# Optimization experiments

Measured on AMD Instinct MI355X. Metric: run time of the kernel, lower is better.

The kernel has to match this reference:

```python
import jax, jax.numpy as jnp
import numpy as np

N = 8192
F = 64
OUT = 64


def setup_inputs() -> dict:
    key = jax.random.key(0)
    k1, k2, k3 = jax.random.split(key, 3)
    adj = jax.random.uniform(k1, (N, N), dtype=jnp.float32)
    features = jax.random.normal(k2, (N, F), dtype=jnp.float32)
    # torch Linear weight: [out_features, in_features*2], xavier_uniform with relu gain
    gain = float(np.sqrt(2.0))
    fan_in, fan_out = 2 * F, OUT
    bound = gain * float(np.sqrt(6.0 / (fan_in + fan_out)))
    W = jax.random.uniform(k3, (OUT, 2 * F), dtype=jnp.float32, minval=-bound, maxval=bound)
    return {"adj": adj, "features": features, "W": W}


def reference(adj, features, W):
    # neigh = (adj @ x) / (rowsum(adj) + 1)   -- dense 2D branch of SageConvLayer
    deg = jnp.sum(adj, axis=1, keepdims=True) + 1.0          # [N, 1]
    neigh = jnp.matmul(adj, features) / deg                   # [N, F]
    data = jnp.concatenate([features, neigh], axis=-1)        # [N, 2F]
    return jnp.matmul(data, W.T)                              # [N, OUT]
```

## Files before the change

### kernel.cpp

```cpp
#include <hip/hip_runtime.h>

#define NN 8192
#define FF 64
#define NOUT 64
#define KS 16
#define KCHUNK (NN / KS)

typedef __bf16 bf16x8 __attribute__((ext_vector_type(8)));
typedef float f32x4 __attribute__((ext_vector_type(4)));

__device__ inline bf16x8 cvt8(float4 a, float4 b) {
    bf16x8 r;
    r[0] = (__bf16)a.x; r[1] = (__bf16)a.y; r[2] = (__bf16)a.z; r[3] = (__bf16)a.w;
    r[4] = (__bf16)b.x; r[5] = (__bf16)b.y; r[6] = (__bf16)b.z; r[7] = (__bf16)b.w;
    return r;
}

__global__ __launch_bounds__(256)
void transpose_kernel(const float* __restrict__ feat, __bf16* __restrict__ featT) {
    __shared__ __bf16 t[64][72];
    int tid = threadIdx.x, blk = blockIdx.x;
    int r = tid >> 2, c0 = (tid & 3) * 16;
    const float* p = feat + (size_t)(blk * 64 + r) * FF + c0;
    float4 v0 = *(const float4*)(p);
    float4 v1 = *(const float4*)(p + 4);
    float4 v2 = *(const float4*)(p + 8);
    float4 v3 = *(const float4*)(p + 12);
    #pragma unroll
    for (int j = 0; j < 4; ++j) {
        t[c0 + 0 + j][r]  = (__bf16)(&v0.x)[j];
        t[c0 + 4 + j][r]  = (__bf16)(&v1.x)[j];
        t[c0 + 8 + j][r]  = (__bf16)(&v2.x)[j];
        t[c0 + 12 + j][r] = (__bf16)(&v3.x)[j];
    }
    __syncthreads();
    int n = tid >> 2, co = (tid & 3) * 16;
    __bf16* dst = featT + (size_t)n * NN + blk * 64 + co;
    *(bf16x8*)dst       = *(const bf16x8*)&t[n][co];
    *(bf16x8*)(dst + 8) = *(const bf16x8*)&t[n][co + 8];
}

__global__ __launch_bounds__(256, 4)
void main_kernel(const float* __restrict__ adj, const __bf16* __restrict__ featT,
                 __bf16* __restrict__ partN, float* __restrict__ partDeg) {
    int tid = threadIdx.x;
    int w = tid >> 6, lane = tid & 63, ln = lane & 15, q = lane >> 4;
    int ks = blockIdx.x & (KS - 1);
    int mt = blockIdx.x >> 4;

    int rowA = mt * 128 + w * 32 + ln;
    const float*  ap0 = adj + (size_t)rowA * NN + ks * KCHUNK + q * 8;
    const float*  ap1 = ap0 + (size_t)16 * NN;
    const __bf16* bp  = featT + (size_t)ln * NN + ks * KCHUNK + q * 8;

    f32x4 acc[2][4], accd[2];
    #pragma unroll
    for (int f = 0; f < 2; ++f) {
        accd[f] = 0;
        #pragma unroll
        for (int t = 0; t < 4; ++t) acc[f][t] = 0;
    }

    bf16x8 ones;
    __bf16 o = (ln == 0) ? (__bf16)1.0f : (__bf16)0.0f;
    #pragma unroll
    for (int i = 0; i < 8; ++i) ones[i] = o;

    #pragma unroll 2
    for (int it = 0; it < KCHUNK / 32; ++it) {
        float4 a0 = *(const float4*)ap0;
        float4 a1 = *(const float4*)(ap0 + 4);
        float4 a2 = *(const float4*)ap1;
        float4 a3 = *(const float4*)(ap1 + 4);
        bf16x8 b0 = *(const bf16x8*)(bp);
        bf16x8 b1 = *(const bf16x8*)(bp + 16 * NN);
        bf16x8 b2 = *(const bf16x8*)(bp + 32 * NN);
        bf16x8 b3 = *(const bf16x8*)(bp + 48 * NN);
        bf16x8 af0 = cvt8(a0, a1);
        bf16x8 af1 = cvt8(a2, a3);
        acc[0][0] = __builtin_amdgcn_mfma_f32_16x16x32_bf16(af0, b0, acc[0][0], 0, 0, 0);
        acc[1][0] = __builtin_amdgcn_mfma_f32_16x16x32_bf16(af1, b0, acc[1][0], 0, 0, 0);
        acc[0][1] = __builtin_amdgcn_mfma_f32_16x16x32_bf16(af0, b1, acc[0][1], 0, 0, 0);
        acc[1][1] = __builtin_amdgcn_mfma_f32_16x16x32_bf16(af1, b1, acc[1][1], 0, 0, 0);
        acc[0][2] = __builtin_amdgcn_mfma_f32_16x16x32_bf16(af0, b2, acc[0][2], 0, 0, 0);
        acc[1][2] = __builtin_amdgcn_mfma_f32_16x16x32_bf16(af1, b2, acc[1][2], 0, 0, 0);
        acc[0][3] = __builtin_amdgcn_mfma_f32_16x16x32_bf16(af0, b3, acc[0][3], 0, 0, 0);
        acc[1][3] = __builtin_amdgcn_mfma_f32_16x16x32_bf16(af1, b3, acc[1][3], 0, 0, 0);
        accd[0] = __builtin_amdgcn_mfma_f32_16x16x32_bf16(af0, ones, accd[0], 0, 0, 0);
        accd[1] = __builtin_amdgcn_mfma_f32_16x16x32_bf16(af1, ones, accd[1], 0, 0, 0);
        ap0 += 32; ap1 += 32; bp += 32;
    }

    #pragma unroll
    for (int f = 0; f < 2; ++f) {
        int grow = mt * 128 + w * 32 + f * 16 + q * 4;
        #pragma unroll
        for (int r = 0; r < 4; ++r) {
            size_t base = ((size_t)(ks << 13) + grow + r) * FF + ln;
            partN[base +  0] = (__bf16)acc[f][0][r];
            partN[base + 16] = (__bf16)acc[f][1][r];
            partN[base + 32] = (__bf16)acc[f][2][r];
            partN[base + 48] = (__bf16)acc[f][3][r];
        }
        if (ln == 0) {
            #pragma unroll
            for (int r = 0; r < 4; ++r)
                partDeg[(ks << 13) + grow + r] = accd[f][r];
        }
    }
}

__global__ __launch_bounds__(256)
void epilogue_kernel(const float* __restrict__ feat, const float* __restrict__ W,
                     const __bf16* __restrict__ partN, const float* __restrict__ partDeg,
                     float* __restrict__ out) {
    __shared__ __bf16 dataB[64][136];
    __shared__ float rdeg[64];
    int tid = threadIdx.x, blk = blockIdx.x;

    if (tid < 64) {
        float s = 0.f;
        #pragma unroll
        for (int ks = 0; ks < KS; ++ks) s += partDeg[(ks << 13) + blk * 64 + tid];
        rdeg[tid] = 1.0f / (s + 1.0f);
    }
    __syncthreads();

    #pragma unroll
    for (int i = 0; i < 2; ++i) {
        int idx = tid + i * 256;
        int r = idx >> 3, c = (idx & 7) * 8;
        float s[8];
        #pragma unroll
        for (int j = 0; j < 8; ++j) s[j] = 0.f;
        #pragma unroll
        for (int ks = 0; ks < KS; ++ks) {
            bf16x8 v = *(const bf16x8*)&partN[((size_t)(ks << 13) + blk * 64 + r) * FF + c];
            #pragma unroll
            for (int j = 0; j < 8; ++j) s[j] += (float)v[j];
        }
        float rd = rdeg[r];
        bf16x8 o;
        #pragma unroll
        for (int j = 0; j < 8; ++j) o[j] = (__bf16)(s[j] * rd);
        *(bf16x8*)&dataB[r][64 + c] = o;
    }
    #pragma unroll
    for (int i = 0; i < 2; ++i) {
        int idx = tid + i * 256;
        int r = idx >> 3, c = (idx & 7) * 8;
        const float* p = feat + (size_t)(blk * 64 + r) * FF + c;
        float4 f0 = *(const float4*)p;
        float4 f1 = *(const float4*)(p + 4);
        *(bf16x8*)&dataB[r][c] = cvt8(f0, f1);
    }
    __syncthreads();

    int w = tid >> 6, lane = tid & 63, ln = lane & 15, q = lane >> 4;
    f32x4 acc[4];
    #pragma unroll
    for (int t = 0; t < 4; ++t) acc[t] = 0;

    #pragma unroll
    for (int kk = 0; kk < 4; ++kk) {
        bf16x8 af = *(const bf16x8*)&dataB[w * 16 + ln][kk * 32 + q * 8];
        #pragma unroll
        for (int t = 0; t < 4; ++t) {
            const float* wp = W + (size_t)(t * 16 + ln) * 128 + kk * 32 + q * 8;
            float4 b0 = *(const float4*)wp;
            float4 b1 = *(const float4*)(wp + 4);
            bf16x8 bf = cvt8(b0, b1);
            acc[t] = __builtin_amdgcn_mfma_f32_16x16x32_bf16(af, bf, acc[t], 0, 0, 0);
        }
    }

    int grow = blk * 64 + w * 16 + q * 4;
    #pragma unroll
    for (int t = 0; t < 4; ++t)
        #pragma unroll
        for (int r = 0; r < 4; ++r)
            out[(size_t)(grow + r) * NOUT + t * 16 + ln] = acc[t][r];
}

extern "C" void kernel_launch(void* const* d_in, const int* in_sizes, int n_in,
                              void* d_out, int out_size, void* d_ws, size_t ws_size,
                              hipStream_t stream) {
    const float* adj  = (const float*)d_in[0];
    const float* feat = (const float*)d_in[1];
    const float* W    = (const float*)d_in[2];
    float* out = (float*)d_out;
    char* ws = (char*)d_ws;

    __bf16* featT   = (__bf16*)ws;
    __bf16* partN   = (__bf16*)(ws + (1 << 20));
    float*  partDeg = (float*)(ws + (1 << 20) + (size_t)KS * NN * FF * 2);

    transpose_kernel<<<NN / 64, 256, 0, stream>>>(feat, featT);
    main_kernel<<<(NN / 128) * KS, 256, 0, stream>>>(adj, featT, partN, partDeg);
    epilogue_kernel<<<NN / 64, 256, 0, stream>>>(feat, W, partN, partDeg, out);
}
```

Baseline: 381.0 us.

## Stage adj tiles through LDS with coalesced row loads before MFMA

The main kernel now loads adj in coalesced 16-lane row segments (64 floats per row per round), converts them to bf16 and writes them into a shared-memory tile. Each wave then reads its MFMA A fragments from LDS instead of each lane fetching strided 32-byte pieces straight from global memory. This targets the poorly coalesced access pattern on the dominant 256 MB adj stream. In exchange it adds two barriers per round and LDS traffic, with no double buffering to hide load latency.

Result: no change. 379.2 us (-0.5%).

```diff
diff --git a/kernel.cpp b/kernel.cpp
--- a/kernel.cpp
+++ b/kernel.cpp
@@ -5,8 +5,11 @@
 #define NOUT 64
 #define KS 16
 #define KCHUNK (NN / KS)
+#define KSTEP 64
+#define ROUNDS (KCHUNK / KSTEP)
 
 typedef __bf16 bf16x8 __attribute__((ext_vector_type(8)));
+typedef __bf16 bf16x4 __attribute__((ext_vector_type(4)));
 typedef float f32x4 __attribute__((ext_vector_type(4)));
 
 __device__ inline bf16x8 cvt8(float4 a, float4 b) {
@@ -43,15 +46,16 @@
 __global__ __launch_bounds__(256, 4)
 void main_kernel(const float* __restrict__ adj, const __bf16* __restrict__ featT,
                  __bf16* __restrict__ partN, float* __restrict__ partDeg) {
+    __shared__ __bf16 at[128][72];
     int tid = threadIdx.x;
     int w = tid >> 6, lane = tid & 63, ln = lane & 15, q = lane >> 4;
     int ks = blockIdx.x & (KS - 1);
     int mt = blockIdx.x >> 4;
 
-    int rowA = mt * 128 + w * 32 + ln;
-    const float*  ap0 = adj + (size_t)rowA * NN + ks * KCHUNK + q * 8;
-    const float*  ap1 = ap0 + (size_t)16 * NN;
-    const __bf16* bp  = featT + (size_t)ln * NN + ks * KCHUNK + q * 8;
+    int sr = tid >> 4;
+    int sc = (tid & 15) * 4;
+    const float* abase = adj + (size_t)(mt * 128 + sr) * NN + ks * KCHUNK + sc;
+    const __bf16* bbase = featT + (size_t)ln * NN + ks * KCHUNK + q * 8;
 
     f32x4 acc[2][4], accd[2];
     #pragma unroll
@@ -66,29 +70,42 @@
     #pragma unroll
     for (int i = 0; i < 8; ++i) ones[i] = o;
 
-    #pragma unroll 2
-    for (int it = 0; it < KCHUNK / 32; ++it) {
-        float4 a0 = *(const float4*)ap0;
-        float4 a1 = *(const float4*)(ap0 + 4);
-        float4 a2 = *(const float4*)ap1;
-        float4 a3 = *(const float4*)(ap1 + 4);
-        bf16x8 b0 = *(const bf16x8*)(bp);
-        bf16x8 b1 = *(const bf16x8*)(bp + 16 * NN);
-        bf16x8 b2 = *(const bf16x8*)(bp + 32 * NN);
-        bf16x8 b3 = *(const bf16x8*)(bp + 48 * NN);
-        bf16x8 af0 = cvt8(a0, a1);
-        bf16x8 af1 = cvt8(a2, a3);
-        acc[0][0] = __builtin_amdgcn_mfma_f32_16x16x32_bf16(af0, b0, acc[0][0], 0, 0, 0);
-        acc[1][0] = __builtin_amdgcn_mfma_f32_16x16x32_bf16(af1, b0, acc[1][0], 0, 0, 0);
-        acc[0][1] = __builtin_amdgcn_mfma_f32_16x16x32_bf16(af0, b1, acc[0][1], 0, 0, 0);
-        acc[1][1] = __builtin_amdgcn_mfma_f32_16x16x32_bf16(af1, b1, acc[1][1], 0, 0, 0);
-        acc[0][2] = __builtin_amdgcn_mfma_f32_16x16x32_bf16(af0, b2, acc[0][2], 0, 0, 0);
-        acc[1][2] = __builtin_amdgcn_mfma_f32_16x16x32_bf16(af1, b2, acc[1][2], 0, 0, 0);
-        acc[0][3] = __builtin_amdgcn_mfma_f32_16x16x32_bf16(af0, b3, acc[0][3], 0, 0, 0);
-        acc[1][3] = __builtin_amdgcn_mfma_f32_16x16x32_bf16(af1, b3, acc[1][3], 0, 0, 0);
-        accd[0] = __builtin_amdgcn_mfma_f32_16x16x32_bf16(af0, ones, accd[0], 0, 0, 0);
-        accd[1] = __builtin_amdgcn_mfma_f32_16x16x32_bf16(af1, ones, accd[1], 0, 0, 0);
-        ap0 += 32; ap1 += 32; bp += 32;
+    for (int rd = 0; rd < ROUNDS; ++rd) {
+        float4 v[8];
+        const float* ap = abase + rd * KSTEP;
+        #pragma unroll
+        for (int i = 0; i < 8; ++i)
+            v[i] = *(const float4*)(ap + (size_t)i * 16 * NN);
+        __syncthreads();
+        #pragma unroll
+        for (int i = 0; i < 8; ++i) {
+            bf16x4 b;
+            b[0] = (__bf16)v[i].x; b[1] = (__bf16)v[i].y;
+            b[2] = (__bf16)v[i].z; b[3] = (__bf16)v[i].w;
+            *(bf16x4*)&at[i * 16 + sr][sc] = b;
+        }
+        __syncthreads();
+
+        #pragma unroll
+        for (int s = 0; s < 2; ++s) {
+            const __bf16* bp = bbase + rd * KSTEP + s * 32;
+            bf16x8 b0 = *(const bf16x8*)(bp);
+            bf16x8 b1 = *(const bf16x8*)(bp + 16 * NN);
+            bf16x8 b2 = *(const bf16x8*)(bp + 32 * NN);
+            bf16x8 b3 = *(const bf16x8*)(bp + 48 * NN);
+            bf16x8 af0 = *(const bf16x8*)&at[w * 32 + ln][s * 32 + q * 8];
+            bf16x8 af1 = *(const bf16x8*)&at[w * 32 + 16 + ln][s * 32 + q * 8];
+            acc[0][0] = __builtin_amdgcn_mfma_f32_16x16x32_bf16(af0, b0, acc[0][0], 0, 0, 0);
+            acc[1][0] = __builtin_amdgcn_mfma_f32_16x16x32_bf16(af1, b0, acc[1][0], 0, 0, 0);
+            acc[0][1] = __builtin_amdgcn_mfma_f32_16x16x32_bf16(af0, b1, acc[0][1], 0, 0, 0);
+            acc[1][1] = __builtin_amdgcn_mfma_f32_16x16x32_bf16(af1, b1, acc[1][1], 0, 0, 0);
+            acc[0][2] = __builtin_amdgcn_mfma_f32_16x16x32_bf16(af0, b2, acc[0][2], 0, 0, 0);
+            acc[1][2] = __builtin_amdgcn_mfma_f32_16x16x32_bf16(af1, b2, acc[1][2], 0, 0, 0);
+            acc[0][3] = __builtin_amdgcn_mfma_f32_16x16x32_bf16(af0, b3, acc[0][3], 0, 0, 0);
+            acc[1][3] = __builtin_amdgcn_mfma_f32_16x16x32_bf16(af1, b3, acc[1][3], 0, 0, 0);
+            accd[0] = __builtin_amdgcn_mfma_f32_16x16x32_bf16(af0, ones, accd[0], 0, 0, 0);
+            accd[1] = __builtin_amdgcn_mfma_f32_16x16x32_bf16(af1, ones, accd[1], 0, 0, 0);
+        }
     }
 
     #pragma unroll
```
